# Kernel optimization log

Hardware: AMD Instinct MI355X
Metric: run time of the kernel (lower is better)

The kernel has to match this reference:

```python
import jax, jax.numpy as jnp
import numpy as np

B, T, DM, H, DH, P = 8, 512, 1024, 16, 64, 3584


def rotate_half(x):
    x1, x2 = x[..., : x.shape[-1] // 2], x[..., x.shape[-1] // 2 :]
    return jnp.concatenate([-x2, x1], axis=-1)


def setup_inputs() -> dict:
    key = jax.random.key(0)
    ks = jax.random.split(key, 16)
    x_new = jax.random.normal(ks[0], (B, T, DM), dtype=jnp.float32)
    # realistic RoPE tables for positions [P, P+T)
    inv_freq = 1.0 / (10000.0 ** (jnp.arange(0, DH, 2, dtype=jnp.float32) / DH))
    pos = jnp.arange(P, P + T, dtype=jnp.float32)
    freqs = pos[:, None] * inv_freq[None, :]  # [T, DH/2]
    emb = jnp.concatenate([freqs, freqs], axis=-1)  # [T, DH]
    rotary_cos = jnp.cos(emb)[None, None]  # [1,1,T,DH]
    rotary_sin = jnp.sin(emb)[None, None]
    past_k = jax.random.normal(ks[1], (B, H, P, DH), dtype=jnp.float32)
    past_v = jax.random.normal(ks[2], (B, H, P, DH), dtype=jnp.float32)
    past_lengths = jax.random.randint(ks[3], (B,), 0, P + 1, dtype=jnp.int32)
    new_token_counts = jax.random.randint(ks[4], (B,), 1, T + 1, dtype=jnp.int32)
    valid_new_mask = jnp.arange(T)[None, :] < new_token_counts[:, None]  # [B,T] bool
    s = 0.02
    Wq = jax.random.normal(ks[5], (DM, DM), dtype=jnp.float32) * s
    Wk = jax.random.normal(ks[6], (DM, DM), dtype=jnp.float32) * s
    Wv = jax.random.normal(ks[7], (DM, DM), dtype=jnp.float32) * s
    Wo = jax.random.normal(ks[8], (DM, DM), dtype=jnp.float32) * s
    bq = jax.random.normal(ks[9], (DM,), dtype=jnp.float32) * s
    bk = jax.random.normal(ks[10], (DM,), dtype=jnp.float32) * s
    bv = jax.random.normal(ks[11], (DM,), dtype=jnp.float32) * s
    bo = jax.random.normal(ks[12], (DM,), dtype=jnp.float32) * s
    return dict(x_new=x_new, rotary_cos=rotary_cos, rotary_sin=rotary_sin,
                past_k=past_k, past_v=past_v, past_lengths=past_lengths,
                valid_new_mask=valid_new_mask, new_token_counts=new_token_counts,
                Wq=Wq, bq=bq, Wk=Wk, bk=bk, Wv=Wv, bv=bv, Wo=Wo, bo=bo)


def reference(x_new, rotary_cos, rotary_sin, past_k, past_v, past_lengths,
              valid_new_mask, new_token_counts, Wq, bq, Wk, bk, Wv, bv, Wo, bo):
    b, t, _ = x_new.shape
    # projections -> [B,H,T,DH]
    def proj(W, bias):
        y = x_new @ W + bias
        return y.reshape(b, t, H, DH).transpose(0, 2, 1, 3)
    q = proj(Wq, bq)
    k_new = proj(Wk, bk)
    v_new = proj(Wv, bv)
    # RoPE on q and new keys
    cos = rotary_cos.astype(q.dtype)
    sin = rotary_sin.astype(q.dtype)
    q = q * cos + rotate_half(q) * sin
    k_new = k_new * cos + rotate_half(k_new) * sin
    # zero out padded new tokens (applied to q, k_new, v_new as in original)
    vmask = valid_new_mask[:, None, :, None].astype(q.dtype)
    q = q * vmask
    k_new = k_new * vmask
    v_new = v_new * vmask
    # trim/mask past cache per sample
    trimmed_past = jnp.clip(past_lengths, 0, P)
    pmask = (jnp.arange(P)[None, :] < trimmed_past[:, None])[:, None, :, None].astype(q.dtype)
    pk = past_k.astype(q.dtype) * pmask
    pv = past_v.astype(q.dtype) * pmask
    k_total = jnp.concatenate([pk, k_new], axis=2)  # [B,H,P+T,DH]
    v_total = jnp.concatenate([pv, v_new], axis=2)
    total_lengths = trimmed_past + new_token_counts  # [B]
    # key validity mask over concatenated axis: positions < total_lengths
    valid_keys = jnp.arange(P + t)[None, :] < total_lengths[:, None]  # [B,S]
    scale = 1.0 / jnp.sqrt(jnp.asarray(DH, dtype=q.dtype))
    scores = jnp.einsum('bhqd,bhkd->bhqk', q, k_total) * scale  # [B,H,T,S]
    neg = jnp.asarray(-1e9, dtype=scores.dtype)
    scores = jnp.where(valid_keys[:, None, None, :], scores, neg)
    attn = jax.nn.softmax(scores, axis=-1)
    out = jnp.einsum('bhqk,bhkd->bhqd', attn, v_total)  # [B,H,T,DH]
    out = out.transpose(0, 2, 1, 3).reshape(b, t, DM)
    out = out @ Wo + bo
    out = out * valid_new_mask[:, :, None].astype(out.dtype)
    return out
```

## Files before the change

kernel.cpp:

```cpp
#include <hip/hip_runtime.h>


typedef unsigned short u16;
typedef unsigned int   u32;
typedef float  f32x4  __attribute__((ext_vector_type(4)));
typedef __bf16 bf16x8 __attribute__((ext_vector_type(8)));

#define DEV static __device__ __forceinline__

constexpr int NP = 3584;

DEV u16 bf16rn(float f){
  u32 u = __float_as_uint(f);
  return (u16)((u + 0x7fffu + ((u >> 16) & 1u)) >> 16);
}
DEV float bf2f(u16 h){ return __uint_as_float((u32)h << 16); }
DEV void split2(float f, u16 &h, u16 &l){ h = bf16rn(f); l = bf16rn(f - bf2f(h)); }

DEV f32x4 mfma16(bf16x8 a, bf16x8 b, f32x4 c){
  return __builtin_amdgcn_mfma_f32_16x16x32_bf16(a, b, c, 0, 0, 0);
}

__global__ __launch_bounds__(256) void k_split_x(const float* __restrict__ x,
                                                 u16* __restrict__ xh, u16* __restrict__ xl){
  int i = blockIdx.x * 256 + threadIdx.x;
  float4 v = ((const float4*)x)[i];
  u16 h0,l0,h1,l1,h2,l2,h3,l3;
  split2(v.x,h0,l0); split2(v.y,h1,l1); split2(v.z,h2,l2); split2(v.w,h3,l3);
  ushort4 hv; hv.x=h0; hv.y=h1; hv.z=h2; hv.w=h3;
  ushort4 lv; lv.x=l0; lv.y=l1; lv.z=l2; lv.w=l3;
  ((ushort4*)xh)[i] = hv; ((ushort4*)xl)[i] = lv;
}

__global__ __launch_bounds__(256) void k_wsplit(const float* __restrict__ w0, const float* __restrict__ w1,
                                                const float* __restrict__ w2, const float* __restrict__ w3,
                                                u16* __restrict__ Wth, u16* __restrict__ Wtl){
  __shared__ float tl[64][65];
  int z = blockIdx.z;
  const float* W = (z==0) ? w0 : (z==1) ? w1 : (z==2) ? w2 : w3;
  u16* oh = Wth + (size_t)z * (1024*1024);
  u16* ol = Wtl + (size_t)z * (1024*1024);
  int n0 = blockIdx.x*64, k0 = blockIdx.y*64;
  int tid = threadIdx.x;
  #pragma unroll
  for (int i=0;i<16;++i){
    int idx = i*256 + tid; int rr = idx >> 6, cc = idx & 63;
    tl[rr][cc] = W[(size_t)(k0+rr)*1024 + n0 + cc];
  }
  __syncthreads();
  #pragma unroll
  for (int i=0;i<16;++i){
    int idx = i*256 + tid; int rr = idx >> 6, cc = idx & 63;
    u16 h,l; split2(tl[cc][rr], h, l);
    size_t o = (size_t)(n0+rr)*1024 + k0 + cc;
    oh[o] = h; ol[o] = l;
  }
}

__global__ __launch_bounds__(256) void k_qkv(
    const u16* __restrict__ xh, const u16* __restrict__ xl,
    const u16* __restrict__ Wth, const u16* __restrict__ Wtl,
    const float* __restrict__ bq, const float* __restrict__ bk, const float* __restrict__ bv,
    const float* __restrict__ rcos, const float* __restrict__ rsin,
    const int* __restrict__ cnts,
    u16* __restrict__ qh, u16* __restrict__ ql,
    u16* __restrict__ kh, u16* __restrict__ vh)
{
  int zi = blockIdx.z;
  int n0 = blockIdx.x * 128, m0 = blockIdx.y * 128;
  int b = m0 >> 9, t0 = m0 & 511;
  int cnt = cnts[b];
  if (t0 >= cnt) return;
  const u16* Bh = Wth + (size_t)zi * (1024*1024);
  const u16* Bl = Wtl + (size_t)zi * (1024*1024);
  const float* bias = (zi==0) ? bq : (zi==1) ? bk : bv;
  u16* oh = (zi==0) ? qh : (zi==1) ? kh : vh;
  u16* ol = ql;

  __shared__ u16 sA[2][128*40];
  __shared__ u16 sB[2][128*40];

  int tid = threadIdx.x, lane = tid & 63, wid = tid >> 6;
  int r = lane & 15, quad = lane >> 4;
  int wm = (wid >> 1) * 64, wn = (wid & 1) * 64;

  const f32x4 fz = {0.f,0.f,0.f,0.f};
  f32x4 acc[4][4];
  #pragma unroll
  for (int i=0;i<4;++i){
    #pragma unroll
    for (int j=0;j<4;++j) acc[i][j] = fz;
  }

  int srow = tid >> 2, sc8 = (tid & 3) * 8;

  for (int kt = 0; kt < 32; ++kt){
    int kb = kt * 32;
    __syncthreads();
    {
      size_t ga  = (size_t)(m0 + srow) * 1024 + kb + sc8;
      size_t gb  = (size_t)(n0 + srow) * 1024 + kb + sc8;
      int lo = srow*40 + sc8, lo2 = lo + 64*40;
      *(uint4*)&sA[0][lo]  = *(const uint4*)&xh[ga];
      *(uint4*)&sA[1][lo]  = *(const uint4*)&xl[ga];
      *(uint4*)&sB[0][lo]  = *(const uint4*)&Bh[gb];
      *(uint4*)&sB[1][lo]  = *(const uint4*)&Bl[gb];
      *(uint4*)&sA[0][lo2] = *(const uint4*)&xh[ga + 64*1024];
      *(uint4*)&sA[1][lo2] = *(const uint4*)&xl[ga + 64*1024];
      *(uint4*)&sB[0][lo2] = *(const uint4*)&Bh[gb + 64*1024];
      *(uint4*)&sB[1][lo2] = *(const uint4*)&Bl[gb + 64*1024];
    }
    __syncthreads();
    bf16x8 ah[4], al[4], bh8[4], bl8[4];
    #pragma unroll
    for (int mf=0; mf<4; ++mf){
      int off = (wm + mf*16 + r)*40 + quad*8;
      ah[mf] = *(const bf16x8*)&sA[0][off];
      al[mf] = *(const bf16x8*)&sA[1][off];
    }
    #pragma unroll
    for (int nf=0; nf<4; ++nf){
      int off = (wn + nf*16 + r)*40 + quad*8;
      bh8[nf] = *(const bf16x8*)&sB[0][off];
      bl8[nf] = *(const bf16x8*)&sB[1][off];
    }
    #pragma unroll
    for (int mf=0; mf<4; ++mf){
      #pragma unroll
      for (int nf=0; nf<4; ++nf){
        acc[mf][nf] = mfma16(ah[mf], bh8[nf], acc[mf][nf]);
        acc[mf][nf] = mfma16(al[mf], bh8[nf], acc[mf][nf]);
        acc[mf][nf] = mfma16(ah[mf], bl8[nf], acc[mf][nf]);
      }
    }
  }

  float vals[4][4][4];
  #pragma unroll
  for (int mf=0;mf<4;++mf){
    #pragma unroll
    for (int nf=0;nf<4;++nf){
      float bb = bias[n0 + wn + nf*16 + r];
      #pragma unroll
      for (int e=0;e<4;++e) vals[mf][nf][e] = acc[mf][nf][e] + bb;
    }
  }
  if (zi < 2){
    #pragma unroll
    for (int mf=0;mf<4;++mf){
      #pragma unroll
      for (int e=0;e<4;++e){
        int t = t0 + wm + mf*16 + quad*4 + e;
        #pragma unroll
        for (int nf=0;nf<2;++nf){
          int d = nf*16 + r;
          float c1 = rcos[t*64 + d],      s1 = rsin[t*64 + d];
          float c2 = rcos[t*64 + d + 32], s2 = rsin[t*64 + d + 32];
          float x1 = vals[mf][nf][e], x2 = vals[mf][nf+2][e];
          vals[mf][nf][e]   = x1*c1 - x2*s1;
          vals[mf][nf+2][e] = x2*c2 + x1*s2;
        }
      }
    }
  }
  #pragma unroll
  for (int mf=0;mf<4;++mf){
    #pragma unroll
    for (int e=0;e<4;++e){
      int t = t0 + wm + mf*16 + quad*4 + e;
      float msk = (t < cnt) ? 1.f : 0.f;
      #pragma unroll
      for (int nf=0;nf<4;++nf){
        int gc = n0 + wn + nf*16 + r;
        int head = gc >> 6, d = gc & 63;
        float v = vals[mf][nf][e] * msk;
        u16 hh, ll; split2(v, hh, ll);
        size_t o = ((size_t)(b*16 + head)*512 + t)*64 + d;
        oh[o] = hh;
        if (zi == 0) ol[o] = ll;
      }
    }
  }
}

__global__ __launch_bounds__(256,3) void k_attn(
    const u16* __restrict__ qh_, const u16* __restrict__ ql_,
    const u16* __restrict__ knh, const u16* __restrict__ vnh,
    const float* __restrict__ pk, const float* __restrict__ pv,
    const int* __restrict__ plen, const int* __restrict__ cnts,
    int S, float* __restrict__ pl, float* __restrict__ pO)
{
  int qt = blockIdx.x, h = blockIdx.y;
  int zb = blockIdx.z;
  int b = zb / S, s = zb - b * S;
  int cnt = cnts[b];
  int q0 = qt * 128;
  if (q0 >= cnt) return;
  int Lp = min(max(plen[b], 0), NP);
  int TL = Lp + cnt;
  int Ln = max(0, TL - NP);
  int jend = min(((Lp + 63) >> 6) << 6, NP);
  int minTLP = min(TL, NP);
  int Zar = max(0, minTLP - jend);
  int npast = jend >> 6, nnew = (Ln + 63) >> 6;
  int Tt = npast + nnew;
  int qsp = (Tt + S - 1) / S;
  int it0 = s * qsp, it1 = min(Tt, it0 + qsp);
  bool hasZ = (s == 0 && Zar > 0);
  if (it0 >= it1 && !hasZ) return;

  __shared__ u16 sK [64*72];
  __shared__ u16 sVT[64*72];
  __shared__ u16 sP [4*32*72];

  int tid = threadIdx.x, lane = tid & 63, wid = tid >> 6;
  int r = lane & 15, quad = lane >> 4;
  int wm0 = wid * 32;

  bf16x8 Qh[2][2], Ql[2][2];
  size_t qbase = ((size_t)(b*16 + h)*512 + q0 + wm0) * 64;
  #pragma unroll
  for (int mf=0;mf<2;++mf){
    #pragma unroll
    for (int ks=0;ks<2;++ks){
      size_t o = qbase + (size_t)(mf*16 + r)*64 + ks*32 + quad*8;
      Qh[mf][ks] = *(const bf16x8*)&qh_[o];
      Ql[mf][ks] = *(const bf16x8*)&ql_[o];
    }
  }

  const f32x4 fz = {0.f,0.f,0.f,0.f};
  f32x4 O[2][4];
  float lsum[2][4];
  #pragma unroll
  for (int mf=0;mf<2;++mf){
    #pragma unroll
    for (int e=0;e<4;++e) lsum[mf][e] = 0.f;
    #pragma unroll
    for (int nf=0;nf<4;++nf) O[mf][nf] = fz;
  }

  const float kscale = 0.125f * 1.44269504088896340736f;
  size_t kvb = (size_t)(b*16 + h) * NP  * 64;
  size_t nb  = (size_t)(b*16 + h) * 512 * 64;
  int sj = tid >> 4, sd0 = (tid & 15) * 4;

  float4 kbuf[4];
  bool nisp = false; int nj0 = 0;
  auto issueK = [&](int itn){
    nisp = itn < npast;
    nj0 = (nisp ? itn : itn - npast) << 6;
    if (nisp){
      #pragma unroll
      for (int i=0;i<4;++i){
        int j = sj + i*16;
        kbuf[i] = *(const float4*)&pk[kvb + (size_t)(nj0 + j)*64 + sd0];
      }
    } else {
      #pragma unroll
      for (int i=0;i<2;++i){
        int j = (tid>>3) + i*32, d0 = (tid & 7)*8;
        kbuf[i] = *(const float4*)&knh[nb + (size_t)(nj0 + j)*64 + d0];
      }
    }
  };
  if (it0 < it1) issueK(it0);

  for (int it = it0; it < it1; ++it){
    bool ispc = nisp; int j0c = nj0;

    if (ispc){
      #pragma unroll
      for (int i=0;i<4;++i){
        int j = sj + i*16;
        float4 kv = kbuf[i];
        if (j0c + j >= Lp){ kv.x=0.f; kv.y=0.f; kv.z=0.f; kv.w=0.f; }
        ushort4 khv; khv.x=bf16rn(kv.x); khv.y=bf16rn(kv.y); khv.z=bf16rn(kv.z); khv.w=bf16rn(kv.w);
        *(ushort4*)&sK[j*72 + sd0] = khv;
      }
    } else {
      #pragma unroll
      for (int i=0;i<2;++i){
        int j = (tid>>3) + i*32, d0 = (tid & 7)*8;
        *(uint4*)&sK[j*72 + d0] = __builtin_bit_cast(uint4, kbuf[i]);
      }
    }

    float4  pvv[4];
    ushort4 vnr[4];
    if (ispc){
      #pragma unroll
      for (int i=0;i<4;++i){
        int j = sj + i*16;
        pvv[i] = *(const float4*)&pv[kvb + (size_t)(j0c + j)*64 + sd0];
      }
    } else {
      #pragma unroll
      for (int i=0;i<4;++i){
        int j = sj + i*16;
        vnr[i] = *(const ushort4*)&vnh[nb + (size_t)(j0c + j)*64 + sd0];
      }
    }

    if (it + 1 < it1) issueK(it + 1);

    __syncthreads();

    f32x4 Sc[2][4];
    #pragma unroll
    for (int mf=0;mf<2;++mf){
      #pragma unroll
      for (int jf=0;jf<4;++jf) Sc[mf][jf] = fz;
    }
    #pragma unroll
    for (int ks=0;ks<2;++ks){
      #pragma unroll
      for (int jf=0;jf<4;++jf){
        int off = (jf*16 + r)*72 + ks*32 + quad*8;
        bf16x8 kbh = *(const bf16x8*)&sK[off];
        #pragma unroll
        for (int mf=0;mf<2;++mf){
          Sc[mf][jf] = mfma16(Qh[mf][ks], kbh, Sc[mf][jf]);
          Sc[mf][jf] = mfma16(Ql[mf][ks], kbh, Sc[mf][jf]);
        }
      }
    }

    if (ispc){
      #pragma unroll
      for (int i=0;i<4;++i){
        int j = sj + i*16;
        float4 vv = pvv[i];
        if (j0c + j >= Lp){ vv.x=0.f; vv.y=0.f; vv.z=0.f; vv.w=0.f; }
        sVT[(sd0+0)*72 + j] = bf16rn(vv.x);
        sVT[(sd0+1)*72 + j] = bf16rn(vv.y);
        sVT[(sd0+2)*72 + j] = bf16rn(vv.z);
        sVT[(sd0+3)*72 + j] = bf16rn(vv.w);
      }
    } else {
      #pragma unroll
      for (int i=0;i<4;++i){
        int j = sj + i*16;
        sVT[(sd0+0)*72 + j] = vnr[i].x;
        sVT[(sd0+1)*72 + j] = vnr[i].y;
        sVT[(sd0+2)*72 + j] = vnr[i].z;
        sVT[(sd0+3)*72 + j] = vnr[i].w;
      }
    }

    int jlim = (ispc ? TL : Ln) - j0c;
    #pragma unroll
    for (int mf=0;mf<2;++mf){
      #pragma unroll
      for (int e=0;e<4;++e){
        int pbase = wid*2304 + (mf*16 + quad*4 + e)*72;
        float ls = 0.f;
        #pragma unroll
        for (int jf=0;jf<4;++jf){
          float sv = Sc[mf][jf][e] * kscale - 4.0f;
          sv = (jf*16 + r < jlim) ? sv : -3.0e38f;
          float pj = exp2f(sv);
          ls += pj;
          sP[pbase + jf*16 + r] = bf16rn(pj);
        }
        lsum[mf][e] += ls;
      }
    }
    __syncthreads();

    #pragma unroll
    for (int ks=0;ks<2;++ks){
      bf16x8 pah[2];
      #pragma unroll
      for (int mf=0;mf<2;++mf){
        int off = wid*2304 + (mf*16 + r)*72 + ks*32 + quad*8;
        pah[mf] = *(const bf16x8*)&sP[off];
      }
      #pragma unroll
      for (int nf=0;nf<4;++nf){
        int off = (nf*16 + r)*72 + ks*32 + quad*8;
        bf16x8 vbh = *(const bf16x8*)&sVT[off];
        #pragma unroll
        for (int mf=0;mf<2;++mf){
          O[mf][nf] = mfma16(pah[mf], vbh, O[mf][nf]);
        }
      }
    }
  }

  int pidx = ((b*16 + h)*4 + qt)*S + s;
  float* plr = pl + (size_t)pidx*128;
  float* po  = pO + (size_t)pidx*8192;
  float zadd = (s == 0) ? (float)Zar * 0.0625f : 0.f;
  #pragma unroll
  for (int mf=0;mf<2;++mf){
    #pragma unroll
    for (int e=0;e<4;++e){
      int row = wm0 + mf*16 + quad*4 + e;
      float l = lsum[mf][e];
      l += __shfl_xor(l, 1);
      l += __shfl_xor(l, 2);
      l += __shfl_xor(l, 4);
      l += __shfl_xor(l, 8);
      if (r == 0) plr[row] = l + zadd;
      #pragma unroll
      for (int nf=0;nf<4;++nf) po[row*64 + nf*16 + r] = O[mf][nf][e];
    }
  }
}

__global__ __launch_bounds__(256) void k_reduce(
    const float* __restrict__ pl, const float* __restrict__ pO,
    const int* __restrict__ plen, const int* __restrict__ cnts,
    int S, u16* __restrict__ aoh, u16* __restrict__ aol)
{
  int qt = blockIdx.x, h = blockIdx.y, b = blockIdx.z;
  int cnt = cnts[b]; int q0 = qt*128;
  if (q0 >= cnt) return;
  int Lp = min(max(plen[b], 0), NP);
  int TL = Lp + cnt;
  int Ln = max(0, TL - NP);
  int jend = min(((Lp + 63) >> 6) << 6, NP);
  int minTLP = min(TL, NP);
  int Zar = max(0, minTLP - jend);
  int npast = jend >> 6, nnew = (Ln + 63) >> 6;
  int Tt = npast + nnew;
  int qsp = (Tt + S - 1) / S;

  int tid = threadIdx.x;
  int row = tid >> 1, c0 = (tid & 1) * 32;
  int base = ((b*16 + h)*4 + qt)*S;

  float L = 0.f;
  float acc[32];
  #pragma unroll
  for (int i=0;i<32;++i) acc[i] = 0.f;
  for (int s2=0;s2<S;++s2){
    bool act = (s2*qsp < Tt) || (s2 == 0 && Zar > 0);
    if (!act) continue;
    L += pl[(size_t)(base+s2)*128 + row];
    const float4* po = (const float4*)(pO + (size_t)(base+s2)*8192 + row*64 + c0);
    #pragma unroll
    for (int i=0;i<8;++i){
      float4 v = po[i];
      acc[4*i+0] += v.x; acc[4*i+1] += v.y; acc[4*i+2] += v.z; acc[4*i+3] += v.w;
    }
  }
  float inv = 1.f / L;
  size_t o = ((size_t)b*512 + q0 + row)*1024 + h*64 + c0;
  #pragma unroll
  for (int i=0;i<8;++i){
    ushort4 hv, lv;
    u16 hh, ll;
    split2(acc[4*i+0]*inv, hh, ll); hv.x=hh; lv.x=ll;
    split2(acc[4*i+1]*inv, hh, ll); hv.y=hh; lv.y=ll;
    split2(acc[4*i+2]*inv, hh, ll); hv.z=hh; lv.z=ll;
    split2(acc[4*i+3]*inv, hh, ll); hv.w=hh; lv.w=ll;
    *(ushort4*)&aoh[o + 4*i] = hv;
    *(ushort4*)&aol[o + 4*i] = lv;
  }
}

__global__ __launch_bounds__(256) void k_oproj(
    const u16* __restrict__ ah_, const u16* __restrict__ al_,
    const u16* __restrict__ Wth, const u16* __restrict__ Wtl,
    const float* __restrict__ bo, const int* __restrict__ cnts,
    float* __restrict__ out)
{
  int n0 = blockIdx.x * 128, m0 = blockIdx.y * 128;
  int b = m0 >> 9, t0 = m0 & 511;
  int cnt = cnts[b];
  int tid = threadIdx.x;
  if (t0 >= cnt){
    float4 z4 = {0.f,0.f,0.f,0.f};
    #pragma unroll
    for (int i=0;i<16;++i){
      int v = tid + i*256;
      int row = v >> 5, c4 = (v & 31) * 4;
      *(float4*)&out[(size_t)(m0+row)*1024 + n0 + c4] = z4;
    }
    return;
  }
  const u16* Bh = Wth + 3ull*1024*1024;
  const u16* Bl = Wtl + 3ull*1024*1024;

  __shared__ u16 sA[2][128*40];
  __shared__ u16 sB[2][128*40];

  int lane = tid & 63, wid = tid >> 6;
  int r = lane & 15, quad = lane >> 4;
  int wm = (wid >> 1) * 64, wn = (wid & 1) * 64;

  const f32x4 fz = {0.f,0.f,0.f,0.f};
  f32x4 acc[4][4];
  #pragma unroll
  for (int i=0;i<4;++i){
    #pragma unroll
    for (int j=0;j<4;++j) acc[i][j] = fz;
  }

  int srow = tid >> 2, sc8 = (tid & 3) * 8;

  for (int kt = 0; kt < 32; ++kt){
    int kb = kt * 32;
    __syncthreads();
    {
      size_t ga  = (size_t)(m0 + srow) * 1024 + kb + sc8;
      size_t gb  = (size_t)(n0 + srow) * 1024 + kb + sc8;
      int lo = srow*40 + sc8, lo2 = lo + 64*40;
      *(uint4*)&sA[0][lo]  = *(const uint4*)&ah_[ga];
      *(uint4*)&sA[1][lo]  = *(const uint4*)&al_[ga];
      *(uint4*)&sB[0][lo]  = *(const uint4*)&Bh[gb];
      *(uint4*)&sB[1][lo]  = *(const uint4*)&Bl[gb];
      *(uint4*)&sA[0][lo2] = *(const uint4*)&ah_[ga + 64*1024];
      *(uint4*)&sA[1][lo2] = *(const uint4*)&al_[ga + 64*1024];
      *(uint4*)&sB[0][lo2] = *(const uint4*)&Bh[gb + 64*1024];
      *(uint4*)&sB[1][lo2] = *(const uint4*)&Bl[gb + 64*1024];
    }
    __syncthreads();
    bf16x8 ah8[4], al8[4], bh8[4], bl8[4];
    #pragma unroll
    for (int mf=0; mf<4; ++mf){
      int off = (wm + mf*16 + r)*40 + quad*8;
      ah8[mf] = *(const bf16x8*)&sA[0][off];
      al8[mf] = *(const bf16x8*)&sA[1][off];
    }
    #pragma unroll
    for (int nf=0; nf<4; ++nf){
      int off = (wn + nf*16 + r)*40 + quad*8;
      bh8[nf] = *(const bf16x8*)&sB[0][off];
      bl8[nf] = *(const bf16x8*)&sB[1][off];
    }
    #pragma unroll
    for (int mf=0; mf<4; ++mf){
      #pragma unroll
      for (int nf=0; nf<4; ++nf){
        acc[mf][nf] = mfma16(ah8[mf], bh8[nf], acc[mf][nf]);
        acc[mf][nf] = mfma16(al8[mf], bh8[nf], acc[mf][nf]);
        acc[mf][nf] = mfma16(ah8[mf], bl8[nf], acc[mf][nf]);
      }
    }
  }

  #pragma unroll
  for (int mf=0;mf<4;++mf){
    #pragma unroll
    for (int e=0;e<4;++e){
      int t = t0 + wm + mf*16 + quad*4 + e;
      float msk = (t < cnt) ? 1.f : 0.f;
      int row = m0 + wm + mf*16 + quad*4 + e;
      #pragma unroll
      for (int nf=0;nf<4;++nf){
        int gc = n0 + wn + nf*16 + r;
        out[(size_t)row*1024 + gc] = (acc[mf][nf][e] + bo[gc]) * msk;
      }
    }
  }
}

extern "C" void kernel_launch(void* const* d_in, const int* in_sizes, int n_in,
                              void* d_out, int out_size, void* d_ws, size_t ws_size,
                              hipStream_t stream) {
  (void)in_sizes; (void)n_in; (void)out_size;
  const float* x    = (const float*)d_in[0];
  const float* rcos = (const float*)d_in[1];
  const float* rsin = (const float*)d_in[2];
  const float* pk   = (const float*)d_in[3];
  const float* pv   = (const float*)d_in[4];
  const int*   plen = (const int*)d_in[5];
  const int*   cnts = (const int*)d_in[7];
  const float* Wq = (const float*)d_in[8];
  const float* bq = (const float*)d_in[9];
  const float* Wk = (const float*)d_in[10];
  const float* bk = (const float*)d_in[11];
  const float* Wv = (const float*)d_in[12];
  const float* bv = (const float*)d_in[13];
  const float* Wo = (const float*)d_in[14];
  const float* bo = (const float*)d_in[15];
  float* out = (float*)d_out;

  char* w = (char*)d_ws;
  const size_t SLOT = 8ull * 1024 * 1024;
  u16* xh  = (u16*)(w + 0*SLOT);
  u16* xl  = (u16*)(w + 1*SLOT);
  u16* Wth = (u16*)(w + 2*SLOT);
  u16* Wtl = (u16*)(w + 3*SLOT);
  u16* qh  = (u16*)(w + 4*SLOT);
  u16* ql  = (u16*)(w + 5*SLOT);
  u16* knh = (u16*)(w + 6*SLOT);
  u16* vnh = (u16*)(w + 7*SLOT);
  float* pl = (float*)(w + 8*SLOT);
  float* pO = (float*)(w + 8*SLOT + (2ull<<20));
  u16* aoh = xh;
  u16* aol = xl;

  size_t used = 8*SLOT + (2ull<<20);
  int S = (int)((ws_size - used) / (16ull<<20));
  if (S > 8) S = 8;
  if (S < 1) S = 1;

  k_split_x<<<dim3(4096), dim3(256), 0, stream>>>(x, xh, xl);
  k_wsplit<<<dim3(16,16,4), dim3(256), 0, stream>>>(Wq, Wk, Wv, Wo, Wth, Wtl);
  k_qkv<<<dim3(8,32,3), dim3(256), 0, stream>>>(xh, xl, Wth, Wtl, bq, bk, bv,
                                                rcos, rsin, cnts,
                                                qh, ql, knh, vnh);
  k_attn<<<dim3(4,16,8*S), dim3(256), 0, stream>>>(qh, ql, knh, vnh,
                                                   pk, pv, plen, cnts, S, pl, pO);
  k_reduce<<<dim3(4,16,8), dim3(256), 0, stream>>>(pl, pO, plen, cnts, S, aoh, aol);
  k_oproj<<<dim3(8,32), dim3(256), 0, stream>>>(aoh, aol, Wth, Wtl, bo, cnts, out);
}
```

Baseline: 590.7 us.

## Pre-transpose past V to bf16, drop low-weight MFMA for Q/K, split K/V prefetch

A new kernel converts the past V cache to bf16 and transposes it once, so the attention kernel loads ready-made V^T tiles. This replaces the per-tile fp32 loads and scattered transposed shared-memory writes. The attention loop now prefetches K and V separately, skips masking on fully valid tiles, and raises the launch-bounds occupancy hint. The Q and K projections drop the third (weight-low) MFMA term, and the manual bf16 rounding is replaced with the hardware conversion. The costs are an extra kernel pass and workspace for V^T, and slightly lower precision for Q and K.

```diff
diff --git a/kernel.cpp b/kernel.cpp
--- a/kernel.cpp
+++ b/kernel.cpp
@@ -10,12 +10,9 @@
 
 constexpr int NP = 3584;
 
-DEV u16 bf16rn(float f){
-  u32 u = __float_as_uint(f);
-  return (u16)((u + 0x7fffu + ((u >> 16) & 1u)) >> 16);
-}
+DEV u16 cvt1(float f){ return __builtin_bit_cast(u16, (__bf16)f); }
 DEV float bf2f(u16 h){ return __uint_as_float((u32)h << 16); }
-DEV void split2(float f, u16 &h, u16 &l){ h = bf16rn(f); l = bf16rn(f - bf2f(h)); }
+DEV void split2(float f, u16 &h, u16 &l){ h = cvt1(f); l = cvt1(f - bf2f(h)); }
 
 DEV f32x4 mfma16(bf16x8 a, bf16x8 b, f32x4 c){
   return __builtin_amdgcn_mfma_f32_16x16x32_bf16(a, b, c, 0, 0, 0);
@@ -54,6 +51,41 @@
     u16 h,l; split2(tl[cc][rr], h, l);
     size_t o = (size_t)(n0+rr)*1024 + k0 + cc;
     oh[o] = h; ol[o] = l;
+  }
+}
+
+__global__ __launch_bounds__(256) void k_vcast(const float* __restrict__ pv,
+                                               const int* __restrict__ plen,
+                                               u16* __restrict__ vpT){
+  int jt = blockIdx.x, h = blockIdx.y, b = blockIdx.z;
+  int Lp = min(max(plen[b],0), NP);
+  int jend = min((Lp+63) & ~63, NP);
+  int j0 = jt*64;
+  if (j0 >= jend) return;
+  __shared__ u16 t[64*72];
+  int tid = threadIdx.x;
+  int j = tid>>2, c4 = tid&3;
+  size_t src = (size_t)(b*16+h)*NP*64 + (size_t)(j0+j)*64;
+  bool live = (j0 + j) < Lp;
+  #pragma unroll
+  for (int k=0;k<4;++k){
+    int d = c4*16 + k*4;
+    float4 v;
+    if (live) v = *(const float4*)&pv[src + d];
+    else { v.x=0.f; v.y=0.f; v.z=0.f; v.w=0.f; }
+    ushort4 hv; hv.x=cvt1(v.x); hv.y=cvt1(v.y); hv.z=cvt1(v.z); hv.w=cvt1(v.w);
+    *(ushort4*)&t[j*72 + d] = hv;
+  }
+  __syncthreads();
+  size_t dst = (size_t)(b*16+h)*64*NP;
+  int vd = tid>>3, vj8 = (tid&7)*8;
+  #pragma unroll
+  for (int k=0;k<2;++k){
+    int d = vd + k*32;
+    u16 tmp[8];
+    #pragma unroll
+    for (int i=0;i<8;++i) tmp[i] = t[(vj8+i)*72 + d];
+    *(uint4*)&vpT[dst + (size_t)d*NP + j0 + vj8] = *(uint4*)tmp;
   }
 }
 
@@ -76,6 +108,7 @@
   const float* bias = (zi==0) ? bq : (zi==1) ? bk : bv;
   u16* oh = (zi==0) ? qh : (zi==1) ? kh : vh;
   u16* ol = ql;
+  bool wlo = (zi == 2);
 
   __shared__ u16 sA[2][128*40];
   __shared__ u16 sB[2][128*40];
@@ -122,7 +155,7 @@
     for (int nf=0; nf<4; ++nf){
       int off = (wn + nf*16 + r)*40 + quad*8;
       bh8[nf] = *(const bf16x8*)&sB[0][off];
-      bl8[nf] = *(const bf16x8*)&sB[1][off];
+      if (wlo) bl8[nf] = *(const bf16x8*)&sB[1][off];
     }
     #pragma unroll
     for (int mf=0; mf<4; ++mf){
@@ -130,7 +163,7 @@
       for (int nf=0; nf<4; ++nf){
         acc[mf][nf] = mfma16(ah[mf], bh8[nf], acc[mf][nf]);
         acc[mf][nf] = mfma16(al[mf], bh8[nf], acc[mf][nf]);
-        acc[mf][nf] = mfma16(ah[mf], bl8[nf], acc[mf][nf]);
+        if (wlo) acc[mf][nf] = mfma16(ah[mf], bl8[nf], acc[mf][nf]);
       }
     }
   }
@@ -183,10 +216,10 @@
   }
 }
 
-__global__ __launch_bounds__(256,3) void k_attn(
+__global__ __launch_bounds__(256,4) void k_attn(
     const u16* __restrict__ qh_, const u16* __restrict__ ql_,
     const u16* __restrict__ knh, const u16* __restrict__ vnh,
-    const float* __restrict__ pk, const float* __restrict__ pv,
+    const float* __restrict__ pk, const u16* __restrict__ vpT,
     const int* __restrict__ plen, const int* __restrict__ cnts,
     int S, float* __restrict__ pl, float* __restrict__ pO)
 {
@@ -199,7 +232,7 @@
   int Lp = min(max(plen[b], 0), NP);
   int TL = Lp + cnt;
   int Ln = max(0, TL - NP);
-  int jend = min(((Lp + 63) >> 6) << 6, NP);
+  int jend = min((Lp + 63) & ~63, NP);
   int minTLP = min(TL, NP);
   int Zar = max(0, minTLP - jend);
   int npast = jend >> 6, nnew = (Ln + 63) >> 6;
@@ -243,68 +276,76 @@
   const float kscale = 0.125f * 1.44269504088896340736f;
   size_t kvb = (size_t)(b*16 + h) * NP  * 64;
   size_t nb  = (size_t)(b*16 + h) * 512 * 64;
+  size_t vtb = (size_t)(b*16 + h) * 64 * NP;
   int sj = tid >> 4, sd0 = (tid & 15) * 4;
-
-  float4 kbuf[4];
-  bool nisp = false; int nj0 = 0;
-  auto issueK = [&](int itn){
-    nisp = itn < npast;
-    nj0 = (nisp ? itn : itn - npast) << 6;
-    if (nisp){
-      #pragma unroll
-      for (int i=0;i<4;++i){
-        int j = sj + i*16;
-        kbuf[i] = *(const float4*)&pk[kvb + (size_t)(nj0 + j)*64 + sd0];
-      }
+  int nj = tid >> 3, nd0 = (tid & 7) * 8;
+  int vd = tid >> 3, vj8 = (tid & 7) * 8;
+
+  float4  kf4[4];
+  uint4   vb2[2];
+  ushort4 vn4[4];
+  bool kp = false, vp2 = false;
+  int kj0 = 0, vj0 = 0;
+
+  auto issueK = [&](int it){
+    kp = it < npast;
+    kj0 = (kp ? it : it - npast) << 6;
+    if (kp){
+      #pragma unroll
+      for (int i=0;i<4;++i)
+        kf4[i] = *(const float4*)&pk[kvb + (size_t)(kj0 + sj + i*16)*64 + sd0];
     } else {
       #pragma unroll
-      for (int i=0;i<2;++i){
-        int j = (tid>>3) + i*32, d0 = (tid & 7)*8;
-        kbuf[i] = *(const float4*)&knh[nb + (size_t)(nj0 + j)*64 + d0];
-      }
+      for (int i=0;i<2;++i)
+        kf4[i] = __builtin_bit_cast(float4,
+                   *(const uint4*)&knh[nb + (size_t)(kj0 + nj + i*32)*64 + nd0]);
     }
   };
-  if (it0 < it1) issueK(it0);
+  auto issueV = [&](int it){
+    vp2 = it < npast;
+    vj0 = (vp2 ? it : it - npast) << 6;
+    if (vp2){
+      #pragma unroll
+      for (int i=0;i<2;++i)
+        vb2[i] = *(const uint4*)&vpT[vtb + (size_t)(vd + i*32)*NP + vj0 + vj8];
+    } else {
+      #pragma unroll
+      for (int i=0;i<4;++i)
+        vn4[i] = *(const ushort4*)&vnh[nb + (size_t)(vj0 + sj + i*16)*64 + sd0];
+    }
+  };
+
+  if (it0 < it1){ issueK(it0); issueV(it0); }
 
   for (int it = it0; it < it1; ++it){
-    bool ispc = nisp; int j0c = nj0;
+    bool ispc = kp; int j0c = kj0;
 
     if (ispc){
-      #pragma unroll
-      for (int i=0;i<4;++i){
-        int j = sj + i*16;
-        float4 kv = kbuf[i];
-        if (j0c + j >= Lp){ kv.x=0.f; kv.y=0.f; kv.z=0.f; kv.w=0.f; }
-        ushort4 khv; khv.x=bf16rn(kv.x); khv.y=bf16rn(kv.y); khv.z=bf16rn(kv.z); khv.w=bf16rn(kv.w);
-        *(ushort4*)&sK[j*72 + sd0] = khv;
+      if (j0c + 64 <= Lp){
+        #pragma unroll
+        for (int i=0;i<4;++i){
+          float4 kv = kf4[i];
+          ushort4 kh4; kh4.x=cvt1(kv.x); kh4.y=cvt1(kv.y); kh4.z=cvt1(kv.z); kh4.w=cvt1(kv.w);
+          *(ushort4*)&sK[(sj + i*16)*72 + sd0] = kh4;
+        }
+      } else {
+        #pragma unroll
+        for (int i=0;i<4;++i){
+          int j = sj + i*16;
+          float4 kv = kf4[i];
+          if (j0c + j >= Lp){ kv.x=0.f; kv.y=0.f; kv.z=0.f; kv.w=0.f; }
+          ushort4 kh4; kh4.x=cvt1(kv.x); kh4.y=cvt1(kv.y); kh4.z=cvt1(kv.z); kh4.w=cvt1(kv.w);
+          *(ushort4*)&sK[j*72 + sd0] = kh4;
+        }
       }
     } else {
       #pragma unroll
-      for (int i=0;i<2;++i){
-        int j = (tid>>3) + i*32, d0 = (tid & 7)*8;
-        *(uint4*)&sK[j*72 + d0] = __builtin_bit_cast(uint4, kbuf[i]);
-      }
-    }
-
-    float4  pvv[4];
-    ushort4 vnr[4];
-    if (ispc){
-      #pragma unroll
-      for (int i=0;i<4;++i){
-        int j = sj + i*16;
-        pvv[i] = *(const float4*)&pv[kvb + (size_t)(j0c + j)*64 + sd0];
-      }
-    } else {
-      #pragma unroll
-      for (int i=0;i<4;++i){
-        int j = sj + i*16;
-        vnr[i] = *(const ushort4*)&vnh[nb + (size_t)(j0c + j)*64 + sd0];
-      }
-    }
+      for (int i=0;i<2;++i)
+        *(uint4*)&sK[(nj + i*32)*72 + nd0] = __builtin_bit_cast(uint4, kf4[i]);
+    }
+    __syncthreads();
 
     if (it + 1 < it1) issueK(it + 1);
-
-    __syncthreads();
 
     f32x4 Sc[2][4];
     #pragma unroll
@@ -326,44 +367,56 @@
       }
     }
 
-    if (ispc){
+    if (vp2){
+      #pragma unroll
+      for (int i=0;i<2;++i)
+        *(uint4*)&sVT[(vd + i*32)*72 + vj8] = vb2[i];
+    } else {
       #pragma unroll
       for (int i=0;i<4;++i){
         int j = sj + i*16;
-        float4 vv = pvv[i];
-        if (j0c + j >= Lp){ vv.x=0.f; vv.y=0.f; vv.z=0.f; vv.w=0.f; }
-        sVT[(sd0+0)*72 + j] = bf16rn(vv.x);
-        sVT[(sd0+1)*72 + j] = bf16rn(vv.y);
-        sVT[(sd0+2)*72 + j] = bf16rn(vv.z);
-        sVT[(sd0+3)*72 + j] = bf16rn(vv.w);
+        sVT[(sd0+0)*72 + j] = vn4[i].x;
+        sVT[(sd0+1)*72 + j] = vn4[i].y;
+        sVT[(sd0+2)*72 + j] = vn4[i].z;
+        sVT[(sd0+3)*72 + j] = vn4[i].w;
+      }
+    }
+    if (it + 1 < it1) issueV(it + 1);
+
+    int jlim = (ispc ? TL : Ln) - j0c;
+    if (jlim >= 64){
+      #pragma unroll
+      for (int mf=0;mf<2;++mf){
+        #pragma unroll
+        for (int e=0;e<4;++e){
+          int pbase = wid*2304 + (mf*16 + quad*4 + e)*72;
+          float ls = 0.f;
+          #pragma unroll
+          for (int jf=0;jf<4;++jf){
+            float pj = exp2f(Sc[mf][jf][e] * kscale - 4.0f);
+            ls += pj;
+            sP[pbase + jf*16 + r] = cvt1(pj);
+          }
+          lsum[mf][e] += ls;
+        }
       }
     } else {
       #pragma unroll
-      for (int i=0;i<4;++i){
-        int j = sj + i*16;
-        sVT[(sd0+0)*72 + j] = vnr[i].x;
-        sVT[(sd0+1)*72 + j] = vnr[i].y;
-        sVT[(sd0+2)*72 + j] = vnr[i].z;
-        sVT[(sd0+3)*72 + j] = vnr[i].w;
-      }
-    }
-
-    int jlim = (ispc ? TL : Ln) - j0c;
-    #pragma unroll
-    for (int mf=0;mf<2;++mf){
-      #pragma unroll
-      for (int e=0;e<4;++e){
-        int pbase = wid*2304 + (mf*16 + quad*4 + e)*72;
-        float ls = 0.f;
+      for (int mf=0;mf<2;++mf){
         #pragma unroll
-        for (int jf=0;jf<4;++jf){
-          float sv = Sc[mf][jf][e] * kscale - 4.0f;
-          sv = (jf*16 + r < jlim) ? sv : -3.0e38f;
-          float pj = exp2f(sv);
-          ls += pj;
-          sP[pbase + jf*16 + r] = bf16rn(pj);
+        for (int e=0;e<4;++e){
+          int pbase = wid*2304 + (mf*16 + quad*4 + e)*72;
+          float ls = 0.f;
+          #pragma unroll
+          for (int jf=0;jf<4;++jf){
+            float sv = Sc[mf][jf][e] * kscale - 4.0f;
+            sv = (jf*16 + r < jlim) ? sv : -3.0e38f;
+            float pj = exp2f(sv);
+            ls += pj;
+            sP[pbase + jf*16 + r] = cvt1(pj);
+          }
+          lsum[mf][e] += ls;
         }
-        lsum[mf][e] += ls;
       }
     }
     __syncthreads();
@@ -420,7 +473,7 @@
   int Lp = min(max(plen[b], 0), NP);
   int TL = Lp + cnt;
   int Ln = max(0, TL - NP);
-  int jend = min(((Lp + 63) >> 6) << 6, NP);
+  int jend = min((Lp + 63) & ~63, NP);
   int minTLP = min(TL, NP);
   int Zar = max(0, minTLP - jend);
   int npast = jend >> 6, nnew = (Ln + 63) >> 6;
@@ -580,32 +633,33 @@
   float* out = (float*)d_out;
 
   char* w = (char*)d_ws;
-  const size_t SLOT = 8ull * 1024 * 1024;
-  u16* xh  = (u16*)(w + 0*SLOT);
-  u16* xl  = (u16*)(w + 1*SLOT);
-  u16* Wth = (u16*)(w + 2*SLOT);
-  u16* Wtl = (u16*)(w + 3*SLOT);
-  u16* qh  = (u16*)(w + 4*SLOT);
-  u16* ql  = (u16*)(w + 5*SLOT);
-  u16* knh = (u16*)(w + 6*SLOT);
-  u16* vnh = (u16*)(w + 7*SLOT);
-  float* pl = (float*)(w + 8*SLOT);
-  float* pO = (float*)(w + 8*SLOT + (2ull<<20));
+  const size_t MB = 1024ull*1024;
+  u16* xh  = (u16*)(w +   0*MB);
+  u16* xl  = (u16*)(w +   8*MB);
+  u16* Wth = (u16*)(w +  16*MB);
+  u16* Wtl = (u16*)(w +  24*MB);
+  u16* qh  = (u16*)(w +  32*MB);
+  u16* ql  = (u16*)(w +  40*MB);
+  u16* knh = (u16*)(w +  48*MB);
+  u16* vnh = (u16*)(w +  56*MB);
+  u16* vpT = (u16*)(w +  64*MB);
+  float* pl = (float*)(w + 120*MB);
+  float* pO = (float*)(w + 122*MB);
   u16* aoh = xh;
   u16* aol = xl;
 
-  size_t used = 8*SLOT + (2ull<<20);
-  int S = (int)((ws_size - used) / (16ull<<20));
+  int S = (int)((ws_size - 122*MB) / (16*MB));
   if (S > 8) S = 8;
   if (S < 1) S = 1;
 
   k_split_x<<<dim3(4096), dim3(256), 0, stream>>>(x, xh, xl);
   k_wsplit<<<dim3(16,16,4), dim3(256), 0, stream>>>(Wq, Wk, Wv, Wo, Wth, Wtl);
+  k_vcast<<<dim3(56,16,8), dim3(256), 0, stream>>>(pv, plen, vpT);
   k_qkv<<<dim3(8,32,3), dim3(256), 0, stream>>>(xh, xl, Wth, Wtl, bq, bk, bv,
                                                 rcos, rsin, cnts,
                                                 qh, ql, knh, vnh);
   k_attn<<<dim3(4,16,8*S), dim3(256), 0, stream>>>(qh, ql, knh, vnh,
-                                                   pk, pv, plen, cnts, S, pl, pO);
+                                                   pk, vpT, plen, cnts, S, pl, pO);
   k_reduce<<<dim3(4,16,8), dim3(256), 0, stream>>>(pl, pO, plen, cnts, S, aoh, aol);
   k_oproj<<<dim3(8,32), dim3(256), 0, stream>>>(aoh, aol, Wth, Wtl, bo, cnts, out);
 }
```

New measurement: 731.2 us. 23.8% more time.
